# Kernel tuning notes

Measured on AMD Instinct MI355X. Metric: run time of the kernel, lower is better.

## Reference

```python
import jax, jax.numpy as jnp
import numpy as np

D_MODEL = 2048
D_HID = 4096
N_EXPERTS = 8
TOP_K = 2
B, S = 2, 2048


def setup_inputs() -> dict:
    key = jax.random.key(0)
    ks = jax.random.split(key, 4)
    x = jax.random.normal(ks[0], (B, S, D_MODEL), dtype=jnp.float32)
    router_w = jax.random.normal(ks[1], (D_MODEL, N_EXPERTS), dtype=jnp.float32) * (D_MODEL ** -0.5)
    w1 = jax.random.normal(ks[2], (N_EXPERTS, D_MODEL, D_HID), dtype=jnp.float32) * (D_MODEL ** -0.5)
    b1 = jnp.zeros((N_EXPERTS, D_HID), dtype=jnp.float32)
    w2 = jax.random.normal(ks[3], (N_EXPERTS, D_HID, D_MODEL), dtype=jnp.float32) * (D_HID ** -0.5)
    b2 = jnp.zeros((N_EXPERTS, D_MODEL), dtype=jnp.float32)
    return {"x": x, "router_w": router_w, "w1": w1, "b1": b1, "w2": w2, "b2": b2}


def reference(x, router_w, w1, b1, w2, b2):
    # x: [B, S, D] -> tokens [T, D]
    Bc, Sc, D = x.shape
    xt = x.reshape(-1, D)                      # [T, D]
    T = xt.shape[0]
    E = w1.shape[0]

    # --- TopKRouter: linear gate -> softmax -> top-k, renormalized weights ---
    logits = xt @ router_w                     # [T, E]
    probs = jax.nn.softmax(logits, axis=-1)    # [T, E]
    weights, indices = jax.lax.top_k(probs, TOP_K)  # [T, K]
    weights = weights / jnp.sum(weights, axis=-1, keepdims=True)

    # Combine weights per (token, expert): sum over k-slots of weight * 1[idx==e]
    combine = jnp.zeros((T, E), dtype=xt.dtype).at[
        jnp.arange(T)[:, None], indices
    ].add(weights)                             # [T, E]

    # --- Expert FFNs: Linear -> GELU (exact, torch default) -> Linear ---
    out = jnp.zeros_like(xt)
    for e in range(E):  # small fixed loop over experts
        h = jax.nn.gelu(xt @ w1[e] + b1[e], approximate=False)  # [T, H]
        y = h @ w2[e] + b2[e]                                   # [T, D]
        out = out + combine[:, e:e + 1] * y

    return out.reshape(Bc, Sc, D)
```

## Files before the change

### kernel.cpp

```cpp
#include <hip/hip_runtime.h>

typedef unsigned short u16;
typedef unsigned int u32;
typedef short bf16x8 __attribute__((ext_vector_type(8)));
typedef float f32x4 __attribute__((ext_vector_type(4)));

#define T_TOK 4096
#define DM 2048
#define DH 4096
#define NE 8
#define MAXSLOT 10240
#define MAXTILE 40

#define OFF_META   128
#define OFF_TILEE  192
#define OFF_TOPE   512
#define OFF_TOPW   33280
#define OFF_SLOTT  66048
#define OFF_UNION  107008
#define OFF_XBF    147968
#define OFF_W1T    16925184ULL
#define OFF_W2T    151142912ULL
#define OFF_Y      285360640ULL
#define OFF_H3     327303680ULL
#define NEED_Y     329400832ULL

__device__ __forceinline__ u16 f2bf(float f) {
  union { float f; u32 u; } v; v.f = f;
  u32 r = v.u + 0x7fffu + ((v.u >> 16) & 1u);
  return (u16)(r >> 16);
}

__device__ __forceinline__ float bf2f(u16 h) {
  union { u32 u; float f; } v; v.u = ((u32)h) << 16; return v.f;
}

__device__ __forceinline__ float f4c(const float4& v, int c) {
  return c == 0 ? v.x : c == 1 ? v.y : c == 2 ? v.z : v.w;
}

__device__ __forceinline__ void gl_lds16(const u16* g, u16* l) {
  typedef __attribute__((address_space(1))) const u32 gu32;
  typedef __attribute__((address_space(3))) u32 lu32;
  __builtin_amdgcn_global_load_lds((gu32*)(const void*)g, (lu32*)(void*)l, 16, 0, 0);
}

__device__ __forceinline__ float gelu_f(float v) {
  float x = v * 0.70710678118654752f;
  float ax = fabsf(x);
  float t = 1.0f / fmaf(0.3275911f, ax, 1.0f);
  float p = t * fmaf(t, fmaf(t, fmaf(t, fmaf(t, 1.061405429f, -1.453152027f),
                                     1.421413741f), -0.284496736f), 0.254829592f);
  float er = 1.0f - p * __expf(-x * x);
  er = copysignf(er, x);
  return 0.5f * v * (1.0f + er);
}

__global__ __launch_bounds__(256) void router_kernel(
    const float* __restrict__ x, const float* __restrict__ rw,
    int* __restrict__ counts, int* __restrict__ top_e, float* __restrict__ top_w)
{
  int wv = threadIdx.x >> 6;
  int lane = threadIdx.x & 63;
  int t = blockIdx.x * 4 + wv;
  if (t >= T_TOK) return;
  const float4* xr = (const float4*)(x + (size_t)t * DM);
  const float4* rw4 = (const float4*)rw;
  float acc[NE];
#pragma unroll
  for (int e = 0; e < NE; ++e) acc[e] = 0.f;
  for (int i = 0; i < 8; ++i) {
    int d4 = i * 64 + lane;
    float4 xv = xr[d4];
#pragma unroll
    for (int j = 0; j < 4; ++j) {
      int d = 4 * d4 + j;
      float4 r0 = rw4[d * 2];
      float4 r1 = rw4[d * 2 + 1];
      float xs = f4c(xv, j);
      acc[0] += xs * r0.x; acc[1] += xs * r0.y; acc[2] += xs * r0.z; acc[3] += xs * r0.w;
      acc[4] += xs * r1.x; acc[5] += xs * r1.y; acc[6] += xs * r1.z; acc[7] += xs * r1.w;
    }
  }
#pragma unroll
  for (int off = 32; off > 0; off >>= 1)
#pragma unroll
    for (int e = 0; e < NE; ++e) acc[e] += __shfl_xor(acc[e], off, 64);
  if (lane == 0) {
    int e0 = 0; float l0 = acc[0];
#pragma unroll
    for (int e = 1; e < NE; ++e) if (acc[e] > l0) { l0 = acc[e]; e0 = e; }
    int e1 = -1; float l1 = -3.0e38f;
#pragma unroll
    for (int e = 0; e < NE; ++e) if (e != e0 && acc[e] > l1) { l1 = acc[e]; e1 = e; }
    float w0 = 1.f / (1.f + expf(l1 - l0));
    float w1 = 1.f - w0;
    top_e[t * 2 + 0] = e0; top_e[t * 2 + 1] = e1;
    top_w[t * 2 + 0] = w0; top_w[t * 2 + 1] = w1;
    atomicAdd(&counts[e0], 1);
    atomicAdd(&counts[e1], 1);
  }
}

__global__ void scan_kernel(int* __restrict__ wsI)
{
  int* counts = wsI;
  int* curs   = wsI + 8;
  int* offs   = wsI + 16;
  int* meta   = wsI + (OFF_META / 4);
  int* tile_e = wsI + (OFF_TILEE / 4);
  int* slot_token = wsI + (OFF_SLOTT / 4);
  float* slot_wt = (float*)(wsI + (OFF_UNION / 4));
  __shared__ int s_off[9];
  if (threadIdx.x == 0) {
    int o = 0;
    for (int e = 0; e < NE; ++e) {
      offs[e] = o; curs[e] = o; s_off[e] = o;
      o += (counts[e] + 255) & ~255;
    }
    offs[8] = o; s_off[8] = o;
    meta[0] = o >> 8;
  }
  __syncthreads();
  int nt = s_off[8] >> 8;
  for (int i = threadIdx.x; i < MAXTILE; i += blockDim.x) {
    int e = -1;
    if (i < nt) {
      for (int j = 0; j < NE; ++j)
        if (i * 256 >= s_off[j] && i * 256 < s_off[j + 1]) e = j;
    }
    tile_e[i] = e;
  }
  for (int i = threadIdx.x; i < MAXSLOT; i += blockDim.x) {
    slot_token[i] = -1;
    slot_wt[i] = 0.f;
  }
}

__global__ void scatter_kernel(const int* __restrict__ top_e, const float* __restrict__ top_w,
                               int* __restrict__ curs, int* __restrict__ slot_token,
                               int* __restrict__ tok_slots, float* __restrict__ slot_wt,
                               int useY)
{
  int t = blockIdx.x * blockDim.x + threadIdx.x;
  if (t >= T_TOK) return;
#pragma unroll
  for (int k = 0; k < 2; ++k) {
    int e = top_e[t * 2 + k];
    int pos = atomicAdd(&curs[e], 1);
    slot_token[pos] = t;
    if (useY) tok_slots[t * 2 + k] = pos;
    else      slot_wt[pos] = top_w[t * 2 + k];
  }
}

__global__ __launch_bounds__(256) void convert_x_kernel(const float* __restrict__ x, u16* __restrict__ xbf)
{
  size_t i = ((size_t)blockIdx.x * 256 + threadIdx.x) * 8;
  float4 a = *(const float4*)(x + i);
  float4 b = *(const float4*)(x + i + 4);
  union { uint4 u; u16 s[8]; } o;
  o.s[0] = f2bf(a.x); o.s[1] = f2bf(a.y); o.s[2] = f2bf(a.z); o.s[3] = f2bf(a.w);
  o.s[4] = f2bf(b.x); o.s[5] = f2bf(b.y); o.s[6] = f2bf(b.z); o.s[7] = f2bf(b.w);
  *(uint4*)(xbf + i) = o.u;
}

__global__ __launch_bounds__(256) void transpose_w_kernel(
    const float* __restrict__ w1, const float* __restrict__ w2,
    u16* __restrict__ w1t, u16* __restrict__ w2t)
{
  __shared__ u16 T_s[4][64][72];
  int bid = blockIdx.x;
  const float* W; u16* Wt; int K, N, k0, n0;
  if (bid < 4096) {
    int e = bid >> 9, r = bid & 511;
    W = w1 + (size_t)e * DM * DH; Wt = w1t + (size_t)e * DM * DH;
    K = DM; N = DH; k0 = (r >> 4) * 64; n0 = (r & 15) * 256;
  } else {
    int b2 = bid - 4096;
    int e = b2 >> 9, r = b2 & 511;
    W = w2 + (size_t)e * DM * DH; Wt = w2t + (size_t)e * DM * DH;
    K = DH; N = DM; k0 = (r >> 3) * 64; n0 = (r & 7) * 256;
  }
  int wv = threadIdx.x >> 6, l = threadIdx.x & 63;
  int nw = n0 + wv * 64;
  const float* src = W + (size_t)k0 * N + nw + l;
  for (int j = 0; j < 8; ++j) {
    float v[8];
#pragma unroll
    for (int i = 0; i < 8; ++i) v[i] = src[(size_t)(j * 8 + i) * N];
    uint4 pk;
    pk.x = f2bf(v[0]) | ((u32)f2bf(v[1]) << 16);
    pk.y = f2bf(v[2]) | ((u32)f2bf(v[3]) << 16);
    pk.z = f2bf(v[4]) | ((u32)f2bf(v[5]) << 16);
    pk.w = f2bf(v[6]) | ((u32)f2bf(v[7]) << 16);
    *(uint4*)&T_s[wv][l][j * 8] = pk;
  }
  __syncthreads();
#pragma unroll
  for (int r2 = 0; r2 < 8; ++r2) {
    int row = r2 * 8 + (l >> 3);
    uint4 vv = *(const uint4*)&T_s[wv][row][(l & 7) * 8];
    *(uint4*)(Wt + (size_t)(nw + row) * K + k0 + (l & 7) * 8) = vv;
  }
}


#define GATE8 asm volatile("s_waitcnt vmcnt(8)" ::: "memory")
#define GATE4 asm volatile("s_waitcnt vmcnt(4)" ::: "memory")
#define GATE0 asm volatile("s_waitcnt vmcnt(0)" ::: "memory")
#define NOGATE ((void)0)
#define NOSTG  ((void)0)
#define NORD   ((void)0)

#define STA(BF, KS, KO) do { \
  gl_lds16(aptr0 + (KO) + (KS) * 32, &A_s[BF][KS][wid * 16][0]);       \
  gl_lds16(aptr1 + (KO) + (KS) * 32, &A_s[BF][KS][128 + wid * 16][0]); } while (0)
#define STB(BF, KS, KO) do { \
  gl_lds16(bptr0 + (KO) + (KS) * 32, &B_s[BF][KS][wid * 16][0]);       \
  gl_lds16(bptr1 + (KO) + (KS) * 32, &B_s[BF][KS][128 + wid * 16][0]); } while (0)

#define RDA(S, BF, KS, MH)                                              \
  _Pragma("unroll")                                                     \
  for (int i_ = 0; i_ < 4; ++i_)                                        \
    S[i_] = *(const bf16x8*)&A_s[BF][KS][wm + ((MH) * 4 + i_) * 16 + lrow][sp8]
#define RDB(S, BF, KS)                                                  \
  _Pragma("unroll")                                                     \
  for (int n_ = 0; n_ < 4; ++n_)                                        \
    S[n_] = *(const bf16x8*)&B_s[BF][KS][wn + n_ * 16 + lrow][sp8]

#define PH(AFC, BFRC, MHc, STG, GATE, ...) do {                         \
  STG;                                                                  \
  GATE;                                                                 \
  __builtin_amdgcn_s_barrier();                                         \
  asm volatile("s_waitcnt lgkmcnt(0)" ::: "memory");                    \
  __builtin_amdgcn_sched_barrier(0);                                    \
  __builtin_amdgcn_s_setprio(1);                                        \
  _Pragma("unroll")                                                     \
  for (int nf = 0; nf < 4; ++nf)                                        \
    _Pragma("unroll")                                                   \
    for (int i = 0; i < 4; ++i)                                         \
      acc[nf][(MHc) * 4 + i] = __builtin_amdgcn_mfma_f32_16x16x32_bf16( \
          BFRC[nf], AFC[i], acc[nf][(MHc) * 4 + i], 0, 0, 0);           \
  __builtin_amdgcn_s_setprio(0);                                        \
  __VA_ARGS__;                                                          \
  __builtin_amdgcn_s_barrier();                                         \
  __builtin_amdgcn_sched_barrier(0);                                    \
} while (0)

template<int MODE, int EPI>
__global__ __launch_bounds__(512) void gemm8p(
    const u16* __restrict__ Wt, const float* __restrict__ bias,
    const u16* __restrict__ Abase,
    u16* __restrict__ Hout, u16* __restrict__ Ybuf, float* __restrict__ Out,
    const int* __restrict__ slot_token, const float* __restrict__ slot_wt,
    const int* __restrict__ tile_e, const int* __restrict__ meta,
    int tile0, int mtc)
{
  constexpr int KD = (MODE == 0) ? DM : DH;
  constexpr int ND = (MODE == 0) ? DH : DM;
  constexpr int NT = ND / 256;

  __shared__ u16 A_s[2][2][256][32];
  __shared__ u16 B_s[2][2][256][32];

  int nwg = gridDim.x;
  int flat = blockIdx.x;
  int q8 = nwg >> 3, rr = nwg & 7;
  int xcd = flat & 7, i0 = flat >> 3;
  int wg = (xcd < rr ? xcd * (q8 + 1) : rr * (q8 + 1) + (xcd - rr) * q8) + i0;
  int mloc = wg / NT;
  int ntile = wg % NT;
  int mt = tile0 + mloc;
  if (mt >= meta[0]) return;
  int e = tile_e[mt];
  int n0 = ntile * 256;

  const int tid = threadIdx.x;
  const int lane = tid & 63;
  const int wid = tid >> 6;
  const int lrow = lane & 15;
  const int g = lane >> 4;
  const int sp8 = (g ^ ((lrow >> 1) & 3)) << 3;
  const int wm = (wid >> 2) << 7;
  const int wn = (wid & 3) << 6;

  const int srow = tid >> 2;
  const int swz = ((tid & 3) ^ ((tid >> 3) & 3)) << 3;

  const u16 *aptr0, *aptr1;
  if (MODE == 0) {
    int t0 = slot_token[mt * 256 + srow];        if (t0 < 0) t0 = 0;
    int t1 = slot_token[mt * 256 + 128 + srow];  if (t1 < 0) t1 = 0;
    aptr0 = Abase + (size_t)t0 * KD + swz;
    aptr1 = Abase + (size_t)t1 * KD + swz;
  } else {
    aptr0 = Abase + (size_t)(mloc * 256 + srow) * KD + swz;
    aptr1 = Abase + (size_t)(mloc * 256 + 128 + srow) * KD + swz;
  }
  const u16* bptr0 = Wt + ((size_t)e * ND + n0 + srow) * KD + swz;
  const u16* bptr1 = bptr0 + (size_t)128 * KD;

  f32x4 acc[4][8] = {};
  bf16x8 afX[4], afY[4], bfrX[4], bfrY[4];

  STA(0, 0, 0);  STB(0, 0, 0);
  STA(0, 1, 0);  STB(0, 1, 0);
  STA(1, 0, 64); STB(1, 0, 64);
  GATE8;
  __builtin_amdgcn_s_barrier();
  __builtin_amdgcn_sched_barrier(0);
  RDA(afX, 0, 0, 0);
  RDB(bfrX, 0, 0);

  constexpr int NKT = KD / 64;
  for (int u = 0; u + 4 <= NKT; u += 2) {
    int ko1 = (u + 1) * 64, ko2 = (u + 2) * 64, ko3 = (u + 3) * 64;
    PH(afX, bfrX, 0, STA(1, 1, ko1), NOGATE, RDA(afY, 0, 0, 1));
    PH(afY, bfrX, 1, STB(1, 1, ko1), GATE8,  RDA(afX, 0, 1, 0); RDB(bfrY, 0, 1));
    PH(afX, bfrY, 0, STA(0, 0, ko2), NOGATE, RDA(afY, 0, 1, 1));
    PH(afY, bfrY, 1, STB(0, 0, ko2), GATE8,  RDA(afX, 1, 0, 0); RDB(bfrX, 1, 0));
    PH(afX, bfrX, 0, STA(0, 1, ko2), NOGATE, RDA(afY, 1, 0, 1));
    PH(afY, bfrX, 1, STB(0, 1, ko2), GATE8,  RDA(afX, 1, 1, 0); RDB(bfrY, 1, 1));
    PH(afX, bfrY, 0, STA(1, 0, ko3), NOGATE, RDA(afY, 1, 1, 1));
    PH(afY, bfrY, 1, STB(1, 0, ko3), GATE8,  RDA(afX, 0, 0, 0); RDB(bfrX, 0, 0));
  }
  {
    int ko1 = (NKT - 1) * 64;
    PH(afX, bfrX, 0, STA(1, 1, ko1), NOGATE, RDA(afY, 0, 0, 1));
    PH(afY, bfrX, 1, STB(1, 1, ko1), GATE8,  RDA(afX, 0, 1, 0); RDB(bfrY, 0, 1));
    PH(afX, bfrY, 0, NOSTG,          NOGATE, RDA(afY, 0, 1, 1));
    PH(afY, bfrY, 1, NOSTG,          GATE4,  RDA(afX, 1, 0, 0); RDB(bfrX, 1, 0));
    PH(afX, bfrX, 0, NOSTG,          NOGATE, RDA(afY, 1, 0, 1));
    PH(afY, bfrX, 1, NOSTG,          GATE0,  RDA(afX, 1, 1, 0); RDB(bfrY, 1, 1));
    PH(afX, bfrY, 0, NOSTG,          NOGATE, RDA(afY, 1, 1, 1));
    PH(afY, bfrY, 1, NOSTG,          NOGATE, NORD);
  }

  const int rb = g << 2;
  float4 bias4[4];
#pragma unroll
  for (int nf = 0; nf < 4; ++nf)
    bias4[nf] = *(const float4*)&bias[e * ND + n0 + wn + nf * 16 + rb];

  if constexpr (MODE == 0) {
#pragma unroll
    for (int mf = 0; mf < 8; ++mf) {
      u16* hp = Hout + (size_t)(mloc * 256 + wm + mf * 16 + lrow) * DH + n0 + wn + rb;
#pragma unroll
      for (int nf = 0; nf < 4; ++nf) {
        float v0 = gelu_f(acc[nf][mf][0] + bias4[nf].x);
        float v1 = gelu_f(acc[nf][mf][1] + bias4[nf].y);
        float v2 = gelu_f(acc[nf][mf][2] + bias4[nf].z);
        float v3 = gelu_f(acc[nf][mf][3] + bias4[nf].w);
        uint2 pk;
        pk.x = f2bf(v0) | ((u32)f2bf(v1) << 16);
        pk.y = f2bf(v2) | ((u32)f2bf(v3) << 16);
        *(uint2*)(hp + nf * 16) = pk;
      }
    }
  } else if constexpr (EPI == 0) {
#pragma unroll
    for (int mf = 0; mf < 8; ++mf) {
      u16* yp = Ybuf + (size_t)(mt * 256 + wm + mf * 16 + lrow) * DM + n0 + wn + rb;
#pragma unroll
      for (int nf = 0; nf < 4; ++nf) {
        float v0 = acc[nf][mf][0] + bias4[nf].x;
        float v1 = acc[nf][mf][1] + bias4[nf].y;
        float v2 = acc[nf][mf][2] + bias4[nf].z;
        float v3 = acc[nf][mf][3] + bias4[nf].w;
        uint2 pk;
        pk.x = f2bf(v0) | ((u32)f2bf(v1) << 16);
        pk.y = f2bf(v2) | ((u32)f2bf(v3) << 16);
        *(uint2*)(yp + nf * 16) = pk;
      }
    }
  } else {
#pragma unroll
    for (int mf = 0; mf < 8; ++mf) {
      int gs = mt * 256 + wm + mf * 16 + lrow;
      int tok = slot_token[gs];
      if (tok < 0) continue;
      float wt = slot_wt[gs];
      float* op = Out + (size_t)tok * DM + n0 + wn + rb;
#pragma unroll
      for (int nf = 0; nf < 4; ++nf) {
        atomicAdd(op + nf * 16 + 0, wt * (acc[nf][mf][0] + bias4[nf].x));
        atomicAdd(op + nf * 16 + 1, wt * (acc[nf][mf][1] + bias4[nf].y));
        atomicAdd(op + nf * 16 + 2, wt * (acc[nf][mf][2] + bias4[nf].z));
        atomicAdd(op + nf * 16 + 3, wt * (acc[nf][mf][3] + bias4[nf].w));
      }
    }
  }
}

__global__ __launch_bounds__(256) void combine_kernel(
    const u16* __restrict__ y, const int* __restrict__ tok_slots,
    const float* __restrict__ top_w, float* __restrict__ out)
{
  int t = blockIdx.x;
  int d = threadIdx.x * 8;
  int s0 = tok_slots[t * 2], s1 = tok_slots[t * 2 + 1];
  float w0 = top_w[t * 2], w1 = top_w[t * 2 + 1];
  union { uint4 u; u16 s[8]; } a, b;
  a.u = *(const uint4*)(y + (size_t)s0 * DM + d);
  b.u = *(const uint4*)(y + (size_t)s1 * DM + d);
  float o[8];
#pragma unroll
  for (int j = 0; j < 8; ++j) o[j] = w0 * bf2f(a.s[j]) + w1 * bf2f(b.s[j]);
  float* op = out + (size_t)t * DM + d;
  *(float4*)op = make_float4(o[0], o[1], o[2], o[3]);
  *(float4*)(op + 4) = make_float4(o[4], o[5], o[6], o[7]);
}

extern "C" void kernel_launch(void* const* d_in, const int* in_sizes, int n_in,
                              void* d_out, int out_size, void* d_ws, size_t ws_size,
                              hipStream_t stream) {
  const float* x  = (const float*)d_in[0];
  const float* rw = (const float*)d_in[1];
  const float* w1 = (const float*)d_in[2];
  const float* b1 = (const float*)d_in[3];
  const float* w2 = (const float*)d_in[4];
  const float* b2 = (const float*)d_in[5];
  float* out = (float*)d_out;
  char* ws = (char*)d_ws;

  int* counts = (int*)ws;
  int* curs   = (int*)(ws + 32);
  int* meta   = (int*)(ws + OFF_META);
  int* tile_e = (int*)(ws + OFF_TILEE);
  int* top_e  = (int*)(ws + OFF_TOPE);
  float* top_w = (float*)(ws + OFF_TOPW);
  int* slot_token = (int*)(ws + OFF_SLOTT);
  int* tok_slots  = (int*)(ws + OFF_UNION);
  float* slot_wt  = (float*)(ws + OFF_UNION);
  u16* xbf = (u16*)(ws + OFF_XBF);
  u16* w1t = (u16*)(ws + OFF_W1T);
  u16* w2t = (u16*)(ws + OFF_W2T);

  const int useY = (ws_size >= NEED_Y) ? 1 : 0;
  u16* ybuf = (u16*)(ws + OFF_Y);
  u16* hbuf = (u16*)(ws + (useY ? OFF_H3 : OFF_Y));

  hipMemsetAsync(ws, 0, 512, stream);
  if (!useY) hipMemsetAsync(d_out, 0, (size_t)out_size * sizeof(float), stream);

  router_kernel<<<T_TOK / 4, 256, 0, stream>>>(x, rw, counts, top_e, top_w);
  scan_kernel<<<1, 256, 0, stream>>>((int*)ws);
  scatter_kernel<<<T_TOK / 256, 256, 0, stream>>>(top_e, top_w, curs, slot_token,
                                                  tok_slots, slot_wt, useY);
  convert_x_kernel<<<T_TOK * DM / (256 * 8), 256, 0, stream>>>(x, xbf);
  transpose_w_kernel<<<8192, 256, 0, stream>>>(w1, w2, w1t, w2t);

  size_t hoff = useY ? OFF_H3 : OFF_Y;
  size_t avail = ws_size > hoff ? ws_size - hoff : (size_t)DH * 512;
  long ch_slots = (long)(avail / (DH * 2));
  ch_slots = (ch_slots / 256) * 256;
  if (ch_slots > MAXSLOT) ch_slots = MAXSLOT;
  if (ch_slots < 256) ch_slots = 256;
  int mtc = (int)(ch_slots / 256);
  int nchunks = (MAXTILE + mtc - 1) / mtc;

  for (int c = 0; c < nchunks; ++c) {
    int tile0 = c * mtc;
    gemm8p<0, 0><<<dim3(mtc * (DH / 256)), 512, 0, stream>>>(
        w1t, b1, xbf, hbuf, nullptr, nullptr, slot_token, slot_wt, tile_e, meta, tile0, mtc);
    if (useY) {
      gemm8p<1, 0><<<dim3(mtc * (DM / 256)), 512, 0, stream>>>(
          w2t, b2, hbuf, nullptr, ybuf, nullptr, slot_token, slot_wt, tile_e, meta, tile0, mtc);
    } else {
      gemm8p<1, 1><<<dim3(mtc * (DM / 256)), 512, 0, stream>>>(
          w2t, b2, hbuf, nullptr, nullptr, out, slot_token, slot_wt, tile_e, meta, tile0, mtc);
    }
  }
  if (useY)
    combine_kernel<<<T_TOK, 256, 0, stream>>>(ybuf, tok_slots, top_w, out);
}
```

Baseline: 786.0 us.

## Simplify GEMM main loop to plain double-buffered schedule with two waves per SIMD

Replaces the hand-tuned eight-phase ping-pong schedule, which split A fragments into halves with register double buffering, with a simpler loop. Each half-K step now reads all A/B fragments from LDS, issues the next global-to-LDS loads, waits, and runs 32 MFMAs. Launch bounds now request 2 blocks per CU to raise occupancy. This gives up fine-grained overlap of LDS reads with MFMAs and relies on occupancy to hide latency, at the cost of register pressure limits and more serialization inside each wave.

```diff
diff --git a/kernel.cpp b/kernel.cpp
--- a/kernel.cpp
+++ b/kernel.cpp
@@ -206,12 +206,7 @@
 }
 
 
-#define GATE8 asm volatile("s_waitcnt vmcnt(8)" ::: "memory")
-#define GATE4 asm volatile("s_waitcnt vmcnt(4)" ::: "memory")
-#define GATE0 asm volatile("s_waitcnt vmcnt(0)" ::: "memory")
-#define NOGATE ((void)0)
-#define NOSTG  ((void)0)
-#define NORD   ((void)0)
+#define GATEN(n) asm volatile("s_waitcnt vmcnt(" #n ")" ::: "memory")
 
 #define STA(BF, KS, KO) do { \
   gl_lds16(aptr0 + (KO) + (KS) * 32, &A_s[BF][KS][wid * 16][0]);       \
@@ -220,18 +215,16 @@
   gl_lds16(bptr0 + (KO) + (KS) * 32, &B_s[BF][KS][wid * 16][0]);       \
   gl_lds16(bptr1 + (KO) + (KS) * 32, &B_s[BF][KS][128 + wid * 16][0]); } while (0)
 
-#define RDA(S, BF, KS, MH)                                              \
+#define TOPRD(BF, KS) do {                                              \
   _Pragma("unroll")                                                     \
-  for (int i_ = 0; i_ < 4; ++i_)                                        \
-    S[i_] = *(const bf16x8*)&A_s[BF][KS][wm + ((MH) * 4 + i_) * 16 + lrow][sp8]
-#define RDB(S, BF, KS)                                                  \
+  for (int i_ = 0; i_ < 8; ++i_)                                        \
+    af[i_] = *(const bf16x8*)&A_s[BF][KS][wm + i_ * 16 + lrow][sp8];    \
   _Pragma("unroll")                                                     \
   for (int n_ = 0; n_ < 4; ++n_)                                        \
-    S[n_] = *(const bf16x8*)&B_s[BF][KS][wn + n_ * 16 + lrow][sp8]
-
-#define PH(AFC, BFRC, MHc, STG, GATE, ...) do {                         \
-  STG;                                                                  \
-  GATE;                                                                 \
+    bfr[n_] = *(const bf16x8*)&B_s[BF][KS][wn + n_ * 16 + lrow][sp8];   \
+} while (0)
+
+#define MFMA32 do {                                                     \
   __builtin_amdgcn_s_barrier();                                         \
   asm volatile("s_waitcnt lgkmcnt(0)" ::: "memory");                    \
   __builtin_amdgcn_sched_barrier(0);                                    \
@@ -239,17 +232,16 @@
   _Pragma("unroll")                                                     \
   for (int nf = 0; nf < 4; ++nf)                                        \
     _Pragma("unroll")                                                   \
-    for (int i = 0; i < 4; ++i)                                         \
-      acc[nf][(MHc) * 4 + i] = __builtin_amdgcn_mfma_f32_16x16x32_bf16( \
-          BFRC[nf], AFC[i], acc[nf][(MHc) * 4 + i], 0, 0, 0);           \
+    for (int mf = 0; mf < 8; ++mf)                                      \
+      acc[nf][mf] = __builtin_amdgcn_mfma_f32_16x16x32_bf16(            \
+          bfr[nf], af[mf], acc[nf][mf], 0, 0, 0);                       \
   __builtin_amdgcn_s_setprio(0);                                        \
-  __VA_ARGS__;                                                          \
   __builtin_amdgcn_s_barrier();                                         \
   __builtin_amdgcn_sched_barrier(0);                                    \
 } while (0)
 
 template<int MODE, int EPI>
-__global__ __launch_bounds__(512) void gemm8p(
+__global__ __launch_bounds__(512, 2) void gemm8p(
     const u16* __restrict__ Wt, const float* __restrict__ bias,
     const u16* __restrict__ Abase,
     u16* __restrict__ Hout, u16* __restrict__ Ybuf, float* __restrict__ Out,
@@ -302,39 +294,33 @@
   const u16* bptr1 = bptr0 + (size_t)128 * KD;
 
   f32x4 acc[4][8] = {};
-  bf16x8 afX[4], afY[4], bfrX[4], bfrY[4];
-
-  STA(0, 0, 0);  STB(0, 0, 0);
-  STA(0, 1, 0);  STB(0, 1, 0);
-  STA(1, 0, 64); STB(1, 0, 64);
-  GATE8;
+  bf16x8 af[8], bfr[4];
+
+  STA(0, 0, 0); STB(0, 0, 0);
+  STA(0, 1, 0); STB(0, 1, 0);
+  GATEN(0);
   __builtin_amdgcn_s_barrier();
   __builtin_amdgcn_sched_barrier(0);
-  RDA(afX, 0, 0, 0);
-  RDB(bfrX, 0, 0);
 
   constexpr int NKT = KD / 64;
-  for (int u = 0; u + 4 <= NKT; u += 2) {
-    int ko1 = (u + 1) * 64, ko2 = (u + 2) * 64, ko3 = (u + 3) * 64;
-    PH(afX, bfrX, 0, STA(1, 1, ko1), NOGATE, RDA(afY, 0, 0, 1));
-    PH(afY, bfrX, 1, STB(1, 1, ko1), GATE8,  RDA(afX, 0, 1, 0); RDB(bfrY, 0, 1));
-    PH(afX, bfrY, 0, STA(0, 0, ko2), NOGATE, RDA(afY, 0, 1, 1));
-    PH(afY, bfrY, 1, STB(0, 0, ko2), GATE8,  RDA(afX, 1, 0, 0); RDB(bfrX, 1, 0));
-    PH(afX, bfrX, 0, STA(0, 1, ko2), NOGATE, RDA(afY, 1, 0, 1));
-    PH(afY, bfrX, 1, STB(0, 1, ko2), GATE8,  RDA(afX, 1, 1, 0); RDB(bfrY, 1, 1));
-    PH(afX, bfrY, 0, STA(1, 0, ko3), NOGATE, RDA(afY, 1, 1, 1));
-    PH(afY, bfrY, 1, STB(1, 0, ko3), GATE8,  RDA(afX, 0, 0, 0); RDB(bfrX, 0, 0));
+  for (int t = 0; t < NKT - 1; ++t) {
+    int buf = t & 1, nb = buf ^ 1, ko = (t + 1) * 64;
+    TOPRD(buf, 0);
+    STA(nb, 0, ko); STB(nb, 0, ko);
+    GATEN(4);
+    MFMA32;
+    TOPRD(buf, 1);
+    STA(nb, 1, ko); STB(nb, 1, ko);
+    GATEN(4);
+    MFMA32;
   }
   {
-    int ko1 = (NKT - 1) * 64;
-    PH(afX, bfrX, 0, STA(1, 1, ko1), NOGATE, RDA(afY, 0, 0, 1));
-    PH(afY, bfrX, 1, STB(1, 1, ko1), GATE8,  RDA(afX, 0, 1, 0); RDB(bfrY, 0, 1));
-    PH(afX, bfrY, 0, NOSTG,          NOGATE, RDA(afY, 0, 1, 1));
-    PH(afY, bfrY, 1, NOSTG,          GATE4,  RDA(afX, 1, 0, 0); RDB(bfrX, 1, 0));
-    PH(afX, bfrX, 0, NOSTG,          NOGATE, RDA(afY, 1, 0, 1));
-    PH(afY, bfrX, 1, NOSTG,          GATE0,  RDA(afX, 1, 1, 0); RDB(bfrY, 1, 1));
-    PH(afX, bfrY, 0, NOSTG,          NOGATE, RDA(afY, 1, 1, 1));
-    PH(afY, bfrY, 1, NOSTG,          NOGATE, NORD);
+    int buf = (NKT - 1) & 1;
+    TOPRD(buf, 0);
+    GATEN(0);
+    MFMA32;
+    TOPRD(buf, 1);
+    MFMA32;
   }
 
   const int rb = g << 2;
```

Result: slower. 821.1 us (+4.5%).

## Switch expert GEMMs to 128-row tiles with triple-buffered LDS pipeline

Applied to the files above, without the earlier changes.

Expert token groups are now padded to multiples of 128 instead of 256, which cuts wasted padding rows in the routed GEMMs. The GEMM kernel moves from 512 threads with 256x256 tiles to 256 threads with 128x256 tiles, two blocks per CU, and a three-stage rotating LDS buffer with 32-wide K steps. The smaller M tile raises the number of tiles and lowers per-block weight reuse, and the workspace offsets and slot limits are recomputed to match.

```diff
diff --git a/kernel.cpp b/kernel.cpp
--- a/kernel.cpp
+++ b/kernel.cpp
@@ -9,21 +9,21 @@
 #define DM 2048
 #define DH 4096
 #define NE 8
-#define MAXSLOT 10240
-#define MAXTILE 40
+#define MAXSLOT 9216
+#define MAXTILE 72
 
 #define OFF_META   128
 #define OFF_TILEE  192
 #define OFF_TOPE   512
 #define OFF_TOPW   33280
 #define OFF_SLOTT  66048
-#define OFF_UNION  107008
-#define OFF_XBF    147968
-#define OFF_W1T    16925184ULL
-#define OFF_W2T    151142912ULL
-#define OFF_Y      285360640ULL
-#define OFF_H3     327303680ULL
-#define NEED_Y     329400832ULL
+#define OFF_UNION  102912
+#define OFF_XBF    139776
+#define OFF_W1T    16916992ULL
+#define OFF_W2T    151134720ULL
+#define OFF_Y      285352448ULL
+#define OFF_H3     323101184ULL
+#define NEED_Y     324149760ULL
 
 __device__ __forceinline__ u16 f2bf(float f) {
   union { float f; u32 u; } v; v.f = f;
@@ -116,18 +116,18 @@
     int o = 0;
     for (int e = 0; e < NE; ++e) {
       offs[e] = o; curs[e] = o; s_off[e] = o;
-      o += (counts[e] + 255) & ~255;
+      o += (counts[e] + 127) & ~127;
     }
     offs[8] = o; s_off[8] = o;
-    meta[0] = o >> 8;
+    meta[0] = o >> 7;
   }
   __syncthreads();
-  int nt = s_off[8] >> 8;
+  int nt = s_off[8] >> 7;
   for (int i = threadIdx.x; i < MAXTILE; i += blockDim.x) {
     int e = -1;
     if (i < nt) {
       for (int j = 0; j < NE; ++j)
-        if (i * 256 >= s_off[j] && i * 256 < s_off[j + 1]) e = j;
+        if (i * 128 >= s_off[j] && i * 128 < s_off[j + 1]) e = j;
     }
     tile_e[i] = e;
   }
@@ -206,28 +206,28 @@
 }
 
 
-#define GATE8 asm volatile("s_waitcnt vmcnt(8)" ::: "memory")
-#define GATE4 asm volatile("s_waitcnt vmcnt(4)" ::: "memory")
-#define GATE0 asm volatile("s_waitcnt vmcnt(0)" ::: "memory")
+#define GATEN(n) asm volatile("s_waitcnt vmcnt(" #n ")" ::: "memory")
 #define NOGATE ((void)0)
 #define NOSTG  ((void)0)
 #define NORD   ((void)0)
 
-#define STA(BF, KS, KO) do { \
-  gl_lds16(aptr0 + (KO) + (KS) * 32, &A_s[BF][KS][wid * 16][0]);       \
-  gl_lds16(aptr1 + (KO) + (KS) * 32, &A_s[BF][KS][128 + wid * 16][0]); } while (0)
-#define STB(BF, KS, KO) do { \
-  gl_lds16(bptr0 + (KO) + (KS) * 32, &B_s[BF][KS][wid * 16][0]);       \
-  gl_lds16(bptr1 + (KO) + (KS) * 32, &B_s[BF][KS][128 + wid * 16][0]); } while (0)
-
-#define RDA(S, BF, KS, MH)                                              \
+#define SA_(PA, KO) do { \
+  gl_lds16(aptr0 + (KO), &PA[wid * 16][0]);        \
+  gl_lds16(aptr1 + (KO), &PA[64 + wid * 16][0]); } while (0)
+#define SB1_(PB, KO) gl_lds16(bptr0 + (KO), &PB[wid * 16][0])
+#define SB2_(PB, KO) do { \
+  gl_lds16(bptr1 + (KO), &PB[64 + wid * 16][0]);   \
+  gl_lds16(bptr2 + (KO), &PB[128 + wid * 16][0]);  \
+  gl_lds16(bptr3 + (KO), &PB[192 + wid * 16][0]); } while (0)
+
+#define RDAF(S, P, H)                                                   \
   _Pragma("unroll")                                                     \
   for (int i_ = 0; i_ < 4; ++i_)                                        \
-    S[i_] = *(const bf16x8*)&A_s[BF][KS][wm + ((MH) * 4 + i_) * 16 + lrow][sp8]
-#define RDB(S, BF, KS)                                                  \
+    S[i_] = *(const bf16x8*)&P[(H) * 64 + i_ * 16 + lrow][sp8]
+#define RDBF(S, P)                                                      \
   _Pragma("unroll")                                                     \
   for (int n_ = 0; n_ < 4; ++n_)                                        \
-    S[n_] = *(const bf16x8*)&B_s[BF][KS][wn + n_ * 16 + lrow][sp8]
+    S[n_] = *(const bf16x8*)&P[wn + n_ * 16 + lrow][sp8]
 
 #define PH(AFC, BFRC, MHc, STG, GATE, ...) do {                         \
   STG;                                                                  \
@@ -249,7 +249,7 @@
 } while (0)
 
 template<int MODE, int EPI>
-__global__ __launch_bounds__(512) void gemm8p(
+__global__ __launch_bounds__(256, 2) void gemm_tb(
     const u16* __restrict__ Wt, const float* __restrict__ bias,
     const u16* __restrict__ Abase,
     u16* __restrict__ Hout, u16* __restrict__ Ybuf, float* __restrict__ Out,
@@ -260,9 +260,10 @@
   constexpr int KD = (MODE == 0) ? DM : DH;
   constexpr int ND = (MODE == 0) ? DH : DM;
   constexpr int NT = ND / 256;
-
-  __shared__ u16 A_s[2][2][256][32];
-  __shared__ u16 B_s[2][2][256][32];
+  constexpr int NK = KD / 32;
+
+  __shared__ u16 A_s[3][128][32];
+  __shared__ u16 B_s[3][256][32];
 
   int nwg = gridDim.x;
   int flat = blockIdx.x;
@@ -282,59 +283,58 @@
   const int lrow = lane & 15;
   const int g = lane >> 4;
   const int sp8 = (g ^ ((lrow >> 1) & 3)) << 3;
-  const int wm = (wid >> 2) << 7;
-  const int wn = (wid & 3) << 6;
+  const int wn = wid << 6;
 
   const int srow = tid >> 2;
   const int swz = ((tid & 3) ^ ((tid >> 3) & 3)) << 3;
 
   const u16 *aptr0, *aptr1;
   if (MODE == 0) {
-    int t0 = slot_token[mt * 256 + srow];        if (t0 < 0) t0 = 0;
-    int t1 = slot_token[mt * 256 + 128 + srow];  if (t1 < 0) t1 = 0;
+    int t0 = slot_token[mt * 128 + srow];       if (t0 < 0) t0 = 0;
+    int t1 = slot_token[mt * 128 + 64 + srow];  if (t1 < 0) t1 = 0;
     aptr0 = Abase + (size_t)t0 * KD + swz;
     aptr1 = Abase + (size_t)t1 * KD + swz;
   } else {
-    aptr0 = Abase + (size_t)(mloc * 256 + srow) * KD + swz;
-    aptr1 = Abase + (size_t)(mloc * 256 + 128 + srow) * KD + swz;
+    aptr0 = Abase + (size_t)(mloc * 128 + srow) * KD + swz;
+    aptr1 = Abase + (size_t)(mloc * 128 + 64 + srow) * KD + swz;
   }
   const u16* bptr0 = Wt + ((size_t)e * ND + n0 + srow) * KD + swz;
-  const u16* bptr1 = bptr0 + (size_t)128 * KD;
+  const u16* bptr1 = bptr0 + (size_t)64 * KD;
+  const u16* bptr2 = bptr0 + (size_t)128 * KD;
+  const u16* bptr3 = bptr0 + (size_t)192 * KD;
 
   f32x4 acc[4][8] = {};
-  bf16x8 afX[4], afY[4], bfrX[4], bfrY[4];
-
-  STA(0, 0, 0);  STB(0, 0, 0);
-  STA(0, 1, 0);  STB(0, 1, 0);
-  STA(1, 0, 64); STB(1, 0, 64);
-  GATE8;
+  bf16x8 afX[4], afY[4], bfrA[4], bfrB[4];
+
+  u16 (*pA0)[32] = A_s[0]; u16 (*pA1)[32] = A_s[1]; u16 (*pA2)[32] = A_s[2];
+  u16 (*pB0)[32] = B_s[0]; u16 (*pB1)[32] = B_s[1]; u16 (*pB2)[32] = B_s[2];
+
+  SA_(pA0, 0); SB1_(pB0, 0); SB2_(pB0, 0);
+  SA_(pA1, 32); SB1_(pB1, 32); SB2_(pB1, 32);
+  GATEN(6);
   __builtin_amdgcn_s_barrier();
   __builtin_amdgcn_sched_barrier(0);
-  RDA(afX, 0, 0, 0);
-  RDB(bfrX, 0, 0);
-
-  constexpr int NKT = KD / 64;
-  for (int u = 0; u + 4 <= NKT; u += 2) {
-    int ko1 = (u + 1) * 64, ko2 = (u + 2) * 64, ko3 = (u + 3) * 64;
-    PH(afX, bfrX, 0, STA(1, 1, ko1), NOGATE, RDA(afY, 0, 0, 1));
-    PH(afY, bfrX, 1, STB(1, 1, ko1), GATE8,  RDA(afX, 0, 1, 0); RDB(bfrY, 0, 1));
-    PH(afX, bfrY, 0, STA(0, 0, ko2), NOGATE, RDA(afY, 0, 1, 1));
-    PH(afY, bfrY, 1, STB(0, 0, ko2), GATE8,  RDA(afX, 1, 0, 0); RDB(bfrX, 1, 0));
-    PH(afX, bfrX, 0, STA(0, 1, ko2), NOGATE, RDA(afY, 1, 0, 1));
-    PH(afY, bfrX, 1, STB(0, 1, ko2), GATE8,  RDA(afX, 1, 1, 0); RDB(bfrY, 1, 1));
-    PH(afX, bfrY, 0, STA(1, 0, ko3), NOGATE, RDA(afY, 1, 1, 1));
-    PH(afY, bfrY, 1, STB(1, 0, ko3), GATE8,  RDA(afX, 0, 0, 0); RDB(bfrX, 0, 0));
+  RDAF(afX, pA0, 0);
+  RDBF(bfrA, pB0);
+
+  for (int t = 0; t < NK - 3; t += 2) {
+    int ko2 = (t + 2) * 32, ko3 = (t + 3) * 32;
+    PH(afX, bfrA, 0, SA_(pA2, ko2); SB1_(pB2, ko2), NOGATE,
+       RDAF(afY, pA0, 1));
+    PH(afY, bfrA, 1, SB2_(pB2, ko2), GATEN(6),
+       RDAF(afX, pA1, 0); RDBF(bfrB, pB1));
+    PH(afX, bfrB, 0, SA_(pA0, ko3); SB1_(pB0, ko3), NOGATE,
+       RDAF(afY, pA1, 1));
+    PH(afY, bfrB, 1, SB2_(pB0, ko3), GATEN(6),
+       RDAF(afX, pA2, 0); RDBF(bfrA, pB2));
+    u16 (*tA)[32] = pA0; pA0 = pA2; pA2 = pA1; pA1 = tA;
+    u16 (*tB)[32] = pB0; pB0 = pB2; pB2 = pB1; pB1 = tB;
   }
   {
-    int ko1 = (NKT - 1) * 64;
-    PH(afX, bfrX, 0, STA(1, 1, ko1), NOGATE, RDA(afY, 0, 0, 1));
-    PH(afY, bfrX, 1, STB(1, 1, ko1), GATE8,  RDA(afX, 0, 1, 0); RDB(bfrY, 0, 1));
-    PH(afX, bfrY, 0, NOSTG,          NOGATE, RDA(afY, 0, 1, 1));
-    PH(afY, bfrY, 1, NOSTG,          GATE4,  RDA(afX, 1, 0, 0); RDB(bfrX, 1, 0));
-    PH(afX, bfrX, 0, NOSTG,          NOGATE, RDA(afY, 1, 0, 1));
-    PH(afY, bfrX, 1, NOSTG,          GATE0,  RDA(afX, 1, 1, 0); RDB(bfrY, 1, 1));
-    PH(afX, bfrY, 0, NOSTG,          NOGATE, RDA(afY, 1, 1, 1));
-    PH(afY, bfrY, 1, NOSTG,          NOGATE, NORD);
+    PH(afX, bfrA, 0, NOSTG, NOGATE, RDAF(afY, pA0, 1));
+    PH(afY, bfrA, 1, NOSTG, GATEN(0), RDAF(afX, pA1, 0); RDBF(bfrB, pB1));
+    PH(afX, bfrB, 0, NOSTG, NOGATE, RDAF(afY, pA1, 1));
+    PH(afY, bfrB, 1, NOSTG, NOGATE, NORD);
   }
 
   const int rb = g << 2;
@@ -346,7 +346,7 @@
   if constexpr (MODE == 0) {
 #pragma unroll
     for (int mf = 0; mf < 8; ++mf) {
-      u16* hp = Hout + (size_t)(mloc * 256 + wm + mf * 16 + lrow) * DH + n0 + wn + rb;
+      u16* hp = Hout + (size_t)(mloc * 128 + mf * 16 + lrow) * DH + n0 + wn + rb;
 #pragma unroll
       for (int nf = 0; nf < 4; ++nf) {
         float v0 = gelu_f(acc[nf][mf][0] + bias4[nf].x);
@@ -362,7 +362,7 @@
   } else if constexpr (EPI == 0) {
 #pragma unroll
     for (int mf = 0; mf < 8; ++mf) {
-      u16* yp = Ybuf + (size_t)(mt * 256 + wm + mf * 16 + lrow) * DM + n0 + wn + rb;
+      u16* yp = Ybuf + (size_t)(mt * 128 + mf * 16 + lrow) * DM + n0 + wn + rb;
 #pragma unroll
       for (int nf = 0; nf < 4; ++nf) {
         float v0 = acc[nf][mf][0] + bias4[nf].x;
@@ -378,7 +378,7 @@
   } else {
 #pragma unroll
     for (int mf = 0; mf < 8; ++mf) {
-      int gs = mt * 256 + wm + mf * 16 + lrow;
+      int gs = mt * 128 + mf * 16 + lrow;
       int tok = slot_token[gs];
       if (tok < 0) continue;
       float wt = slot_wt[gs];
@@ -453,23 +453,23 @@
   transpose_w_kernel<<<8192, 256, 0, stream>>>(w1, w2, w1t, w2t);
 
   size_t hoff = useY ? OFF_H3 : OFF_Y;
-  size_t avail = ws_size > hoff ? ws_size - hoff : (size_t)DH * 512;
+  size_t avail = ws_size > hoff ? ws_size - hoff : (size_t)DH * 256;
   long ch_slots = (long)(avail / (DH * 2));
-  ch_slots = (ch_slots / 256) * 256;
+  ch_slots = (ch_slots / 128) * 128;
   if (ch_slots > MAXSLOT) ch_slots = MAXSLOT;
-  if (ch_slots < 256) ch_slots = 256;
-  int mtc = (int)(ch_slots / 256);
+  if (ch_slots < 128) ch_slots = 128;
+  int mtc = (int)(ch_slots / 128);
   int nchunks = (MAXTILE + mtc - 1) / mtc;
 
   for (int c = 0; c < nchunks; ++c) {
     int tile0 = c * mtc;
-    gemm8p<0, 0><<<dim3(mtc * (DH / 256)), 512, 0, stream>>>(
+    gemm_tb<0, 0><<<dim3(mtc * (DH / 256)), 256, 0, stream>>>(
         w1t, b1, xbf, hbuf, nullptr, nullptr, slot_token, slot_wt, tile_e, meta, tile0, mtc);
     if (useY) {
-      gemm8p<1, 0><<<dim3(mtc * (DM / 256)), 512, 0, stream>>>(
+      gemm_tb<1, 0><<<dim3(mtc * (DM / 256)), 256, 0, stream>>>(
           w2t, b2, hbuf, nullptr, ybuf, nullptr, slot_token, slot_wt, tile_e, meta, tile0, mtc);
     } else {
-      gemm8p<1, 1><<<dim3(mtc * (DM / 256)), 512, 0, stream>>>(
+      gemm_tb<1, 1><<<dim3(mtc * (DM / 256)), 256, 0, stream>>>(
           w2t, b2, hbuf, nullptr, nullptr, out, slot_token, slot_wt, tile_e, meta, tile0, mtc);
     }
   }
```

After: 740.5 us. 5.8% less time.
